# Kernel optimization log

Hardware: AMD Instinct MI355X
Metric: run time of the kernel (lower is better)

The kernel has to match this reference:

```python
import jax, jax.numpy as jnp
import numpy as np

B, S, D, H = 128, 512, 256, 256


def _lstm_cell(Wih, Whh, b, x_t, h, c):
    # PyTorch LSTM gate order: i, f, g, o. b = b_ih + b_hh (mathematically equivalent).
    z = x_t @ Wih.T + h @ Whh.T + b  # [B, 4H]
    i, f, g, o = jnp.split(z, 4, axis=-1)
    i = jax.nn.sigmoid(i)
    f = jax.nn.sigmoid(f)
    g = jnp.tanh(g)
    o = jax.nn.sigmoid(o)
    c = f * c + i * g
    h = o * jnp.tanh(c)
    return h, c


def setup_inputs() -> dict:
    key = jax.random.key(0)
    ks = jax.random.split(key, 12)
    s = 1.0 / np.sqrt(H)
    f32 = jnp.float32
    return {
        "x": jax.random.normal(ks[0], (B, S, D), f32),
        "enc_Wih": jax.random.uniform(ks[1], (4 * H, D), f32, -s, s),
        "enc_Whh": jax.random.uniform(ks[2], (4 * H, H), f32, -s, s),
        "enc_b": jax.random.uniform(ks[3], (4 * H,), f32, -s, s),
        "dec_Wih": jax.random.uniform(ks[4], (4 * H, D), f32, -s, s),
        "dec_Whh": jax.random.uniform(ks[5], (4 * H, H), f32, -s, s),
        "dec_b": jax.random.uniform(ks[6], (4 * H,), f32, -s, s),
        "W1_w": jax.random.uniform(ks[7], (H, H), f32, -s, s),
        "W1_b": jax.random.uniform(ks[8], (H,), f32, -s, s),
        "W2_w": jax.random.uniform(ks[9], (H, H), f32, -s, s),
        "W2_b": jax.random.uniform(ks[10], (H,), f32, -s, s),
        "vt_w": jax.random.uniform(ks[11], (H,), f32, -s, s),
    }


def reference(x, enc_Wih, enc_Whh, enc_b, dec_Wih, dec_Whh, dec_b,
              W1_w, W1_b, W2_w, W2_b, vt_w):
    b_, s_, d_ = x.shape
    h0 = jnp.zeros((b_, H), x.dtype)
    c0 = jnp.zeros((b_, H), x.dtype)

    # ---- encoder LSTM over time ----
    def enc_step(carry, x_t):
        h, c = carry
        h, c = _lstm_cell(enc_Wih, enc_Whh, enc_b, x_t, h, c)
        return (h, c), h

    (h, c), enc_out = jax.lax.scan(enc_step, (h0, c0), jnp.swapaxes(x, 0, 1))
    enc_out = jnp.swapaxes(enc_out, 0, 1)  # [B, S, H]

    # W1(encoder_outputs) is loop-invariant; compute once (same math as original)
    enc_proj = enc_out @ W1_w.T + W1_b  # [B, S, H]

    # ---- pointer decode loop ----
    def dec_step(carry, _):
        h, c, din = carry
        h, c = _lstm_cell(dec_Wih, dec_Whh, dec_b, din, h, c)
        q = h @ W2_w.T + W2_b  # [B, H]
        u = jnp.einsum('bsh,h->bs', jnp.tanh(enc_proj + q[:, None, :]), vt_w)
        probs = jax.nn.softmax(u, axis=1)  # [B, S]
        din = jnp.einsum('bs,bsh->bh', probs, enc_out)
        return (h, c, din), probs

    din0 = jnp.zeros((b_, d_), x.dtype)
    _, probs_seq = jax.lax.scan(dec_step, (h, c, din0), None, length=s_)
    return jnp.swapaxes(probs_seq, 0, 1)  # [B, S, S]
```

## Files before the change

kernel.cpp:

```cpp
#include <hip/hip_runtime.h>
#include <hip/hip_fp16.h>

typedef _Float16 h2_t __attribute__((ext_vector_type(2)));
typedef unsigned int u32x4 __attribute__((ext_vector_type(4)));

#define KEXP 2.8853900817779268f

#define BARRIER() do { \
    asm volatile("s_waitcnt lgkmcnt(0)" ::: "memory"); \
    __builtin_amdgcn_s_barrier(); \
    asm volatile("" ::: "memory"); \
} while (0)

__device__ __forceinline__ float fdot2(unsigned int a, unsigned int b, float c) {
#if __has_builtin(__builtin_amdgcn_fdot2)
    return __builtin_amdgcn_fdot2(__builtin_bit_cast(h2_t, a), __builtin_bit_cast(h2_t, b), c, false);
#else
    h2_t ha = __builtin_bit_cast(h2_t, a), hb = __builtin_bit_cast(h2_t, b);
    return c + (float)ha[0]*(float)hb[0] + (float)ha[1]*(float)hb[1];
#endif
}

__device__ __forceinline__ float dot4(u32x4 a, u32x4 b, float c) {
    c = fdot2(a[0], b[0], c); c = fdot2(a[1], b[1], c);
    c = fdot2(a[2], b[2], c); c = fdot2(a[3], b[3], c);
    return c;
}

__device__ __forceinline__ unsigned int pk16(float a, float b) {
    auto h = __builtin_amdgcn_cvt_pkrtz(a, b);
    return __builtin_bit_cast(unsigned int, h);
}

__device__ __forceinline__ float rcp_(float x) {
#if __has_builtin(__builtin_amdgcn_rcpf)
    return __builtin_amdgcn_rcpf(x);
#else
    return 1.0f / x;
#endif
}

__device__ __forceinline__ float sigm(float x) { return rcp_(1.0f + __expf(-x)); }
__device__ __forceinline__ float tanh_(float x) {
    float e = __expf(2.0f * x);
    return 1.0f - 2.0f * rcp_(e + 1.0f);
}

__device__ __forceinline__ unsigned int rcp1p2exp(unsigned int s) {
    __half2 e = h2exp2(__builtin_bit_cast(__half2, s));
    __half2 d = __hadd2(e, __float2half2_rn(1.0f));
    return __builtin_bit_cast(unsigned int, h2rcp(d));
}
__device__ __forceinline__ unsigned int hadd2u(unsigned int a, unsigned int b) {
    return __builtin_bit_cast(unsigned int,
        __hadd2(__builtin_bit_cast(__half2, a), __builtin_bit_cast(__half2, b)));
}

__device__ __forceinline__ void st_u32(unsigned int* p, unsigned int v) {
    __hip_atomic_store(p, v, __ATOMIC_RELAXED, __HIP_MEMORY_SCOPE_AGENT);
}
__device__ __forceinline__ unsigned int ld_u32(const unsigned int* p) {
    return __hip_atomic_load(p, __ATOMIC_RELAXED, __HIP_MEMORY_SCOPE_AGENT);
}
__device__ __forceinline__ float ld_f32(const unsigned int* p) {
    return __builtin_bit_cast(float, ld_u32(p));
}
__device__ __forceinline__ float h2f_lo(unsigned int v) {
    return __half2float(__ushort_as_half((unsigned short)(v & 0xffffu)));
}
__device__ __forceinline__ float h2f_hi(unsigned int v) {
    return __half2float(__ushort_as_half((unsigned short)(v >> 16)));
}

__global__ void init_flags_kernel(unsigned int* flags) {
    flags[threadIdx.x * 32] = 0u;
}

__global__ __launch_bounds__(256) void prep_kernel(
    const float* __restrict__ encWhh, const float* __restrict__ decWih,
    const float* __restrict__ decWhh, const float* __restrict__ W2w,
    u32x4* __restrict__ We8, u32x4* __restrict__ Wi8, u32x4* __restrict__ Wh8, u32x4* __restrict__ W28)
{
    int id = blockIdx.x * 256 + threadIdx.x;
    if (id < 3 * 32768) {
        int mat = id >> 15, local = id & 32767;
        int j = local & 1023, k8 = local >> 10;
        const float* src = mat == 0 ? encWhh : (mat == 1 ? decWih : decWhh);
        u32x4* dst = mat == 0 ? We8 : (mat == 1 ? Wi8 : Wh8);
        const float* p = src + (size_t)j * 256 + k8 * 8;
        float4 a = *(const float4*)p; float4 c = *(const float4*)(p + 4);
        u32x4 v; v[0] = pk16(a.x, a.y); v[1] = pk16(a.z, a.w);
        v[2] = pk16(c.x, c.y); v[3] = pk16(c.z, c.w);
        dst[k8 * 1024 + j] = v;
    } else {
        int local = id - 3 * 32768;
        if (local < 8192) {
            int m = local & 255, k8 = local >> 8;
            const float* p = W2w + (size_t)m * 256 + k8 * 8;
            float4 a = *(const float4*)p; float4 c = *(const float4*)(p + 4);
            u32x4 v; v[0] = pk16(a.x, a.y); v[1] = pk16(a.z, a.w);
            v[2] = pk16(c.x, c.y); v[3] = pk16(c.z, c.w);
            W28[k8 * 256 + m] = v;
        }
    }
}

template<int A_IS_F16, int TR_OUT>
__global__ __launch_bounds__(256) void gemm_kernel(
    const void* __restrict__ A_, const float* __restrict__ Bw,
    const float* __restrict__ bias, unsigned short* __restrict__ C, int N, float scale)
{
    __shared__ float As[16][68];
    __shared__ float Bs[16][132];
    const int t = threadIdx.x;
    const int row0 = blockIdx.y * 64, col0 = blockIdx.x * 128;
    const int ty = t >> 4, tx = t & 15;
    const int lm = t & 63, lkq = t >> 6;
    const int ln = t & 127, lkq2 = t >> 7;
    float acc[4][8] = {};
    for (int k0 = 0; k0 < 256; k0 += 16) {
        float4 av;
        if constexpr (A_IS_F16) {
            const unsigned short* A = (const unsigned short*)A_;
            uint2 ha = *(const uint2*)(A + (size_t)(row0 + lm) * 256 + k0 + lkq * 4);
            h2_t h0 = __builtin_bit_cast(h2_t, ha.x);
            h2_t h1 = __builtin_bit_cast(h2_t, ha.y);
            av = make_float4((float)h0[0], (float)h0[1], (float)h1[0], (float)h1[1]);
        } else {
            av = *(const float4*)((const float*)A_ + (size_t)(row0 + lm) * 256 + k0 + lkq * 4);
        }
        const float* bp = Bw + (size_t)(col0 + ln) * 256 + k0 + lkq2 * 8;
        float4 bv0 = *(const float4*)bp;
        float4 bv1 = *(const float4*)(bp + 4);
        __syncthreads();
        As[lkq * 4 + 0][lm] = av.x;
        As[lkq * 4 + 1][lm] = av.y;
        As[lkq * 4 + 2][lm] = av.z;
        As[lkq * 4 + 3][lm] = av.w;
        Bs[lkq2 * 8 + 0][ln] = bv0.x;
        Bs[lkq2 * 8 + 1][ln] = bv0.y;
        Bs[lkq2 * 8 + 2][ln] = bv0.z;
        Bs[lkq2 * 8 + 3][ln] = bv0.w;
        Bs[lkq2 * 8 + 4][ln] = bv1.x;
        Bs[lkq2 * 8 + 5][ln] = bv1.y;
        Bs[lkq2 * 8 + 6][ln] = bv1.z;
        Bs[lkq2 * 8 + 7][ln] = bv1.w;
        __syncthreads();
        #pragma unroll
        for (int kk = 0; kk < 16; ++kk) {
            float4 a = *(float4*)&As[kk][ty * 4];
            float4 b0 = *(float4*)&Bs[kk][tx * 8];
            float4 b1 = *(float4*)&Bs[kk][tx * 8 + 4];
            float ar[4] = {a.x, a.y, a.z, a.w};
            float br[8] = {b0.x, b0.y, b0.z, b0.w, b1.x, b1.y, b1.z, b1.w};
            #pragma unroll
            for (int i = 0; i < 4; ++i)
                #pragma unroll
                for (int j = 0; j < 8; ++j)
                    acc[i][j] = fmaf(ar[i], br[j], acc[i][j]);
        }
    }
    float bv[8];
    #pragma unroll
    for (int j = 0; j < 8; ++j) bv[j] = bias[col0 + tx * 8 + j];
    #pragma unroll
    for (int i = 0; i < 4; ++i) {
        unsigned int w0 = pk16((acc[i][0] + bv[0]) * scale, (acc[i][1] + bv[1]) * scale);
        unsigned int w1 = pk16((acc[i][2] + bv[2]) * scale, (acc[i][3] + bv[3]) * scale);
        unsigned int w2 = pk16((acc[i][4] + bv[4]) * scale, (acc[i][5] + bv[5]) * scale);
        unsigned int w3 = pk16((acc[i][6] + bv[6]) * scale, (acc[i][7] + bv[7]) * scale);
        uint4 val = make_uint4(w0, w1, w2, w3);
        if constexpr (TR_OUT) {
            int rr = row0 + ty * 4 + i;
            int bb = rr >> 9, s = rr & 511;
            int c8 = (col0 >> 3) + tx;
            ((uint4*)C)[(size_t)bb * 16384 + (size_t)c8 * 512 + s] = val;
        } else {
            *(uint4*)(C + (size_t)(row0 + ty * 4 + i) * N + col0 + tx * 8) = val;
        }
    }
}

__global__ __launch_bounds__(1024) void encoder_kernel(
    const unsigned short* __restrict__ Xproj, const u32x4* __restrict__ We8,
    float* __restrict__ hfin, float* __restrict__ cfin,
    unsigned short* __restrict__ enc_h, unsigned int* __restrict__ encT)
{
    const int b = blockIdx.x, t = threadIdx.x;
    __shared__ __align__(16) float zs[1024];
    __shared__ __align__(16) unsigned int hh2[128];
    if (t < 128) hh2[t] = 0u;
    float c_reg = 0.f, hprev = 0.f, hcur = 0.f;
    __syncthreads();
    const unsigned short* xp = Xproj + (size_t)b * 512 * 1024 + t;
    for (int step = 0; step < 512; ++step) {
        float acc = __half2float(__ushort_as_half(__builtin_nontemporal_load(xp)));
        #pragma unroll 8
        for (int k8 = 0; k8 < 32; ++k8) {
            u32x4 wv = We8[k8 * 1024 + t];
            u32x4 hv = *(const u32x4*)&hh2[k8 * 4];
            acc = dot4(wv, hv, acc);
        }
        zs[t] = acc;
        __syncthreads();
        if (t < 256) {
            float ig = sigm(zs[t]), fg = sigm(zs[t + 256]);
            float gg = tanh_(zs[t + 512]), og = sigm(zs[t + 768]);
            c_reg = fg * c_reg + ig * gg;
            float h = og * tanh_(c_reg);
            float hnb = __shfl_down(h, 1);
            if (!(t & 1)) hh2[t >> 1] = pk16(h, hnb);
            __builtin_nontemporal_store(__half_as_ushort(__float2half_rn(h)),
                                        enc_h + (size_t)(b * 512 + step) * 256 + t);
            if (step & 1) {
                int s2 = step >> 1;
                encT[(size_t)b * 65536 + (size_t)((s2 >> 2) * 256 + t) * 4 + (s2 & 3)] = pk16(hprev, h);
            }
            hprev = h; hcur = h;
        }
        __syncthreads();
        xp += 1024;
    }
    if (t < 256) { hfin[b * 256 + t] = hcur; cfin[b * 256 + t] = c_reg; }
}

__global__ __launch_bounds__(1024) void decoder_kernel(
    const u32x4* __restrict__ Wi8, const u32x4* __restrict__ Wh8, const u32x4* __restrict__ W28,
    const float* __restrict__ dec_b, const float* __restrict__ W2b, const float* __restrict__ vtw,
    const float* __restrict__ hfin, const float* __restrict__ cfin,
    const u32x4* __restrict__ projT, const u32x4* __restrict__ encT,
    unsigned int* __restrict__ xgate, unsigned int* __restrict__ xdin,
    unsigned int* __restrict__ xsum, unsigned int* __restrict__ flags,
    float* __restrict__ out)
{
    const int blk = blockIdx.x;
    const int b = blk & 127, r = blk >> 7;
    const int t = threadIdx.x;
    const int lane = t & 63, w = t >> 6;

    __shared__ __align__(16) float zs[1024];
    __shared__ __align__(16) unsigned int hh2[128];
    __shared__ __align__(16) unsigned int din2[128];
    __shared__ __align__(16) unsigned int qp2[128];
    __shared__ __align__(16) unsigned int mv2u[128];
    __shared__ __align__(16) unsigned int p2u[128];
    __shared__ float wreds[16];
    __shared__ float svtS, rsS;

    const int fo_me = (b * 2 + r) * 32, fo_pr = (b * 2 + (1 - r)) * 32;
    const int go_me = (b * 2 + r) * 256, go_pr = (b * 2 + (1 - r)) * 256;

    float c_reg = (t < 256) ? cfin[b * 256 + t] : 0.f;
    const float bja = (t < 256) ? dec_b[r * 512 + t] : 0.f;
    const float bjb = (t < 256) ? dec_b[r * 512 + 256 + t] : 0.f;
    const float w2b_r = (t < 256) ? W2b[t] : 0.f;
    if (t < 128) { din2[t] = 0u; mv2u[t] = pk16(-2.f * vtw[2 * t], -2.f * vtw[2 * t + 1]); }
    if (t < 256) zs[t] = vtw[t];
    __syncthreads();
    if (t < 64) {
        float v = zs[t] + zs[t + 64] + zs[t + 128] + zs[t + 192];
        #pragma unroll
        for (int off = 1; off < 64; off <<= 1) v += __shfl_xor(v, off);
        if (t == 0) svtS = v;
    }
    if (t < 256) {
        float h0 = hfin[b * 256 + t];
        float hnb = __shfl_down(h0, 1);
        if (!(t & 1)) hh2[t >> 1] = pk16(h0, hnb);
    }
    __syncthreads();
    const float svt = svtS;

    const int jl = t & 511, kh = t >> 9;
    const u32x4* wp = (kh ? Wh8 : Wi8) + (r * 512 + jl);
    const unsigned int* vls = kh ? (const unsigned int*)hh2 : (const unsigned int*)din2;
    const int hF = t & 255, slF = t >> 8;
    const int sl4 = t >> 2, qr = t & 3;
    const int s_g = r * 256 + sl4;
    const u32x4* pD = projT + (size_t)b * 16384 + (size_t)(qr * 8) * 512 + s_g;
    const u32x4* fD = encT + (size_t)b * 16384 + (size_t)(r * 32 + slF * 8) * 256 + hF;
    float* outp = out + (size_t)b * 262144;

    for (int step = 0; step < 512; ++step) {
        float acc = 0.f;
        #pragma unroll 8
        for (int k8 = 0; k8 < 32; ++k8) {
            u32x4 wv = wp[k8 * 1024];
            u32x4 hv = *(const u32x4*)&vls[k8 * 4];
            acc = dot4(wv, hv, acc);
        }
        zs[t] = acc;
        BARRIER();
        unsigned int myg = 0u;
        if (t < 256) {
            float z_a = bja + zs[t] + zs[t + 512];
            float z_b = bjb + zs[t + 256] + zs[t + 768];
            float ga, gb;
            if (r == 0) { ga = sigm(z_a); gb = sigm(z_b); }
            else        { ga = tanh_(z_a); gb = sigm(z_b); }
            myg = (unsigned int)__half_as_ushort(__float2half_rn(ga)) |
                  ((unsigned int)__half_as_ushort(__float2half_rn(gb)) << 16);
            st_u32(&xgate[go_me + t], myg);
            asm volatile("s_waitcnt vmcnt(0)" ::: "memory");
        }
        BARRIER();
        if (t == 0) {
            unsigned int T = (unsigned)(2 * step + 1);
            st_u32(&flags[fo_me], T);
            while (ld_u32(&flags[fo_pr]) < T) __builtin_amdgcn_s_sleep(1);
        }
        BARRIER();
        if (t < 256) {
            unsigned int og = ld_u32(&xgate[go_pr + t]);
            float la = h2f_lo(myg), lb = h2f_hi(myg);
            float oa = h2f_lo(og),  ob = h2f_hi(og);
            float gi, gf, gg, go_;
            if (r == 0) { gi = la; gf = lb; gg = oa; go_ = ob; }
            else        { gg = la; go_ = lb; gi = oa; gf = ob; }
            c_reg = gf * c_reg + gi * gg;
            float h = go_ * tanh_(c_reg);
            float hnb = __shfl_down(h, 1);
            if (!(t & 1)) hh2[t >> 1] = pk16(h, hnb);
        }
        BARRIER();
        {
            float qa = 0.f;
            #pragma unroll
            for (int i = 0; i < 8; ++i) {
                int k8 = slF * 8 + i;
                u32x4 wv = W28[k8 * 256 + hF];
                u32x4 hv = *(const u32x4*)&hh2[k8 * 4];
                qa = dot4(wv, hv, qa);
            }
            zs[t] = qa;
        }
        BARRIER();
        if (t < 256) {
            float q = (w2b_r + zs[t] + zs[t + 256] + zs[t + 512] + zs[t + 768]) * KEXP;
            float qnx = __shfl_down(q, 1);
            if (!(t & 1)) qp2[t >> 1] = pk16(q, qnx);
        }
        BARRIER();
        float e;
        u32x4 fv[8];
        {
            float up = 0.f;
            #pragma unroll 4
            for (int i = 0; i < 8; ++i) {
                u32x4 pv = pD[i * 512];
                int c = qr * 8 + i;
                u32x4 qh = *(const u32x4*)&qp2[c * 4];
                u32x4 mv = *(const u32x4*)&mv2u[c * 4];
                up = fdot2(mv[0], rcp1p2exp(hadd2u(pv[0], qh[0])), up);
                up = fdot2(mv[1], rcp1p2exp(hadd2u(pv[1], qh[1])), up);
                up = fdot2(mv[2], rcp1p2exp(hadd2u(pv[2], qh[2])), up);
                up = fdot2(mv[3], rcp1p2exp(hadd2u(pv[3], qh[3])), up);
            }
            up += __shfl_xor(up, 1);
            up += __shfl_xor(up, 2);
            e = __expf(up + svt);
            #pragma unroll
            for (int j = 0; j < 8; ++j) fv[j] = fD[j * 256];
            float enx = __shfl_down(e, 4);
            if (!(t & 7)) p2u[t >> 3] = pk16(e, enx);
            float ws = e;
            #pragma unroll
            for (int off = 1; off < 64; off <<= 1) ws += __shfl_xor(ws, off);
            if (lane == 0) wreds[w] = ws;
        }
        BARRIER();
        {
            float fa = 0.f;
            #pragma unroll
            for (int j = 0; j < 8; ++j) {
                u32x4 ev = fv[j];
                u32x4 pw = *(const u32x4*)&p2u[(slF * 8 + j) * 4];
                fa = dot4(ev, pw, fa);
            }
            zs[t] = fa;
        }
        BARRIER();
        float dpart = 0.f;
        if (t < 256) {
            dpart = zs[t] + zs[t + 256] + zs[t + 512] + zs[t + 768];
            st_u32(&xdin[go_me + t], __builtin_bit_cast(unsigned int, dpart));
            asm volatile("s_waitcnt vmcnt(0)" ::: "memory");
        }
        BARRIER();
        if (t == 0) {
            float ls = 0.f;
            #pragma unroll
            for (int k = 0; k < 16; ++k) ls += wreds[k];
            ls *= 0.25f;
            st_u32(&xsum[fo_me], __builtin_bit_cast(unsigned int, ls));
            asm volatile("s_waitcnt vmcnt(0)" ::: "memory");
            unsigned int T = (unsigned)(2 * step + 2);
            st_u32(&flags[fo_me], T);
            while (ld_u32(&flags[fo_pr]) < T) __builtin_amdgcn_s_sleep(1);
            float lr = __builtin_bit_cast(float, ld_u32(&xsum[fo_pr]));
            rsS = rcp_(ls + lr);
        }
        BARRIER();
        {
            float rs = rsS;
            if (t < 256) {
                float drem = __builtin_bit_cast(float, ld_u32(&xdin[go_pr + t]));
                float dval = (dpart + drem) * rs;
                float dnx = __shfl_down(dval, 1);
                if (!(t & 1)) din2[t >> 1] = pk16(dval, dnx);
            }
            if ((t & 3) == 0) outp[(size_t)step * 512 + s_g] = e * rs;
        }
        BARRIER();
    }
}

extern "C" void kernel_launch(void* const* d_in, const int* in_sizes, int n_in,
                              void* d_out, int out_size, void* d_ws, size_t ws_size,
                              hipStream_t stream) {
    const float* x      = (const float*)d_in[0];
    const float* encWih = (const float*)d_in[1];
    const float* encWhh = (const float*)d_in[2];
    const float* enc_b  = (const float*)d_in[3];
    const float* decWih = (const float*)d_in[4];
    const float* decWhh = (const float*)d_in[5];
    const float* dec_bp = (const float*)d_in[6];
    const float* W1w    = (const float*)d_in[7];
    const float* W1b    = (const float*)d_in[8];
    const float* W2w    = (const float*)d_in[9];
    const float* W2bp   = (const float*)d_in[10];
    const float* vtw    = (const float*)d_in[11];

    char* ws = (char*)d_ws;
    u32x4* We8 = (u32x4*)(ws);
    u32x4* Wi8 = (u32x4*)(ws + 524288);
    u32x4* Wh8 = (u32x4*)(ws + 1048576);
    u32x4* W28 = (u32x4*)(ws + 1572864);
    unsigned short* enc_h = (unsigned short*)(ws + 1703936);
    unsigned int*   encT  = (unsigned int*)(ws + 35258368);
    unsigned short* projT = (unsigned short*)(ws + 68812800);
    float* hfin = (float*)(ws + 102367232);
    float* cfin = (float*)(ws + 102498304);

    unsigned int* flags = (unsigned int*)(ws + 1703936);
    unsigned int* xsum  = (unsigned int*)(ws + 1703936 + 32768);
    unsigned int* xgate = (unsigned int*)(ws + 1703936 + 65536);
    unsigned int* xdin  = (unsigned int*)(ws + 1703936 + 65536 + 262144);

    unsigned short* Xproj = (unsigned short*)d_out;

    prep_kernel<<<416, 256, 0, stream>>>(encWhh, decWih, decWhh, W2w, We8, Wi8, Wh8, W28);
    gemm_kernel<0, 0><<<dim3(8, 1024), 256, 0, stream>>>(x, encWih, enc_b, Xproj, 1024, 1.0f);
    encoder_kernel<<<128, 1024, 0, stream>>>(Xproj, We8, hfin, cfin, enc_h, (unsigned int*)encT);
    gemm_kernel<1, 1><<<dim3(2, 1024), 256, 0, stream>>>(enc_h, W1w, W1b, projT, 256, KEXP);
    init_flags_kernel<<<1, 256, 0, stream>>>(flags);
    decoder_kernel<<<256, 1024, 0, stream>>>(Wi8, Wh8, W28, dec_bp, W2bp, vtw,
                                             hfin, cfin, (const u32x4*)projT, (const u32x4*)encT,
                                             xgate, xdin, xsum, flags, (float*)d_out);
}
```

Baseline: 13.86 ms.

## Split encoder LSTM across two cooperating blocks per batch with flag exchange

The encoder now runs two workgroups per batch element. Each owns half of the gate outputs, and each thread reduces half of the hidden dimension, with partial sums combined in shared memory. The two blocks trade activated gate halves through global memory every step, using per-step flags and spin-waits, and split the enc_h and encT output writes between them. This halves the per-block weight streaming and per-step matvec latency of the serial recurrence. In exchange it adds a cross-block global handshake on every timestep and depends on both blocks being co-resident.

```diff
diff --git a/kernel.cpp b/kernel.cpp
--- a/kernel.cpp
+++ b/kernel.cpp
@@ -184,44 +184,79 @@
 __global__ __launch_bounds__(1024) void encoder_kernel(
     const unsigned short* __restrict__ Xproj, const u32x4* __restrict__ We8,
     float* __restrict__ hfin, float* __restrict__ cfin,
-    unsigned short* __restrict__ enc_h, unsigned int* __restrict__ encT)
+    unsigned short* __restrict__ enc_h, unsigned int* __restrict__ encT,
+    unsigned int* __restrict__ xg, unsigned int* __restrict__ eflags)
 {
-    const int b = blockIdx.x, t = threadIdx.x;
+    const int blk = blockIdx.x;
+    const int b = blk & 127, r = blk >> 7;
+    const int t = threadIdx.x;
     __shared__ __align__(16) float zs[1024];
     __shared__ __align__(16) unsigned int hh2[128];
     if (t < 128) hh2[t] = 0u;
     float c_reg = 0.f, hprev = 0.f, hcur = 0.f;
     __syncthreads();
-    const unsigned short* xp = Xproj + (size_t)b * 512 * 1024 + t;
+
+    const int jl = t & 511, kh = t >> 9;
+    const u32x4* wp = We8 + (size_t)(kh * 16) * 1024 + r * 512 + jl;
+    const unsigned short* xp = Xproj + (size_t)b * 524288 + r * 512 + jl;
+    const int fo_me = (b * 2 + r) * 32, fo_pr = (b * 2 + (1 - r)) * 32;
+    unsigned int* xg_me = xg + (b * 2 + r) * 512;
+    const unsigned int* xg_pr = xg + (b * 2 + (1 - r)) * 512;
+
     for (int step = 0; step < 512; ++step) {
-        float acc = __half2float(__ushort_as_half(__builtin_nontemporal_load(xp)));
+        float acc = (kh == 0)
+            ? __half2float(__ushort_as_half(__builtin_nontemporal_load(xp + (size_t)step * 1024)))
+            : 0.f;
         #pragma unroll 8
-        for (int k8 = 0; k8 < 32; ++k8) {
-            u32x4 wv = We8[k8 * 1024 + t];
-            u32x4 hv = *(const u32x4*)&hh2[k8 * 4];
+        for (int i = 0; i < 16; ++i) {
+            u32x4 wv = wp[i * 1024];
+            u32x4 hv = *(const u32x4*)&hh2[(kh * 16 + i) * 4];
             acc = dot4(wv, hv, acc);
         }
         zs[t] = acc;
-        __syncthreads();
+        BARRIER();
+        float ga = 0.f, gb = 0.f;
         if (t < 256) {
-            float ig = sigm(zs[t]), fg = sigm(zs[t + 256]);
-            float gg = tanh_(zs[t + 512]), og = sigm(zs[t + 768]);
-            c_reg = fg * c_reg + ig * gg;
-            float h = og * tanh_(c_reg);
+            float z_a = zs[t] + zs[t + 512];
+            float z_b = zs[t + 256] + zs[t + 768];
+            if (r == 0) { ga = sigm(z_a); gb = sigm(z_b); }
+            else        { ga = tanh_(z_a); gb = sigm(z_b); }
+            st_u32(&xg_me[t], __builtin_bit_cast(unsigned int, ga));
+            st_u32(&xg_me[256 + t], __builtin_bit_cast(unsigned int, gb));
+            asm volatile("s_waitcnt vmcnt(0)" ::: "memory");
+        }
+        BARRIER();
+        if (t == 0) {
+            unsigned int T = (unsigned)(step + 1);
+            st_u32(&eflags[fo_me], T);
+            while (ld_u32(&eflags[fo_pr]) < T) __builtin_amdgcn_s_sleep(1);
+        }
+        BARRIER();
+        if (t < 256) {
+            float oa = ld_f32(&xg_pr[t]);
+            float ob = ld_f32(&xg_pr[256 + t]);
+            float gi, gf, gg, go_;
+            if (r == 0) { gi = ga; gf = gb; gg = oa; go_ = ob; }
+            else        { gg = ga; go_ = gb; gi = oa; gf = ob; }
+            c_reg = gf * c_reg + gi * gg;
+            float h = go_ * tanh_(c_reg);
             float hnb = __shfl_down(h, 1);
             if (!(t & 1)) hh2[t >> 1] = pk16(h, hnb);
-            __builtin_nontemporal_store(__half_as_ushort(__float2half_rn(h)),
-                                        enc_h + (size_t)(b * 512 + step) * 256 + t);
-            if (step & 1) {
-                int s2 = step >> 1;
-                encT[(size_t)b * 65536 + (size_t)((s2 >> 2) * 256 + t) * 4 + (s2 & 3)] = pk16(hprev, h);
+            if (r == 0) {
+                __builtin_nontemporal_store(__half_as_ushort(__float2half_rn(h)),
+                                            enc_h + (size_t)(b * 512 + step) * 256 + t);
+            } else {
+                if (step & 1) {
+                    int s2 = step >> 1;
+                    encT[(size_t)b * 65536 + (size_t)((s2 >> 2) * 256 + t) * 4 + (s2 & 3)] = pk16(hprev, h);
+                }
+                hprev = h;
             }
-            hprev = h; hcur = h;
-        }
-        __syncthreads();
-        xp += 1024;
-    }
-    if (t < 256) { hfin[b * 256 + t] = hcur; cfin[b * 256 + t] = c_reg; }
+            hcur = h;
+        }
+        BARRIER();
+    }
+    if (r == 0 && t < 256) { hfin[b * 256 + t] = hcur; cfin[b * 256 + t] = c_reg; }
 }
 
 __global__ __launch_bounds__(1024) void decoder_kernel(
@@ -447,11 +482,16 @@
     unsigned int* xgate = (unsigned int*)(ws + 1703936 + 65536);
     unsigned int* xdin  = (unsigned int*)(ws + 1703936 + 65536 + 262144);
 
+    unsigned int* eflags = (unsigned int*)(ws + 68812800);
+    unsigned int* exg    = (unsigned int*)(ws + 68812800 + 32768);
+
     unsigned short* Xproj = (unsigned short*)d_out;
 
     prep_kernel<<<416, 256, 0, stream>>>(encWhh, decWih, decWhh, W2w, We8, Wi8, Wh8, W28);
     gemm_kernel<0, 0><<<dim3(8, 1024), 256, 0, stream>>>(x, encWih, enc_b, Xproj, 1024, 1.0f);
-    encoder_kernel<<<128, 1024, 0, stream>>>(Xproj, We8, hfin, cfin, enc_h, (unsigned int*)encT);
+    init_flags_kernel<<<1, 256, 0, stream>>>(eflags);
+    encoder_kernel<<<256, 1024, 0, stream>>>(Xproj, We8, hfin, cfin, enc_h, (unsigned int*)encT,
+                                             exg, eflags);
     gemm_kernel<1, 1><<<dim3(2, 1024), 256, 0, stream>>>(enc_h, W1w, W1b, projT, 256, KEXP);
     init_flags_kernel<<<1, 256, 0, stream>>>(flags);
     decoder_kernel<<<256, 1024, 0, stream>>>(Wi8, Wh8, W28, dec_bp, W2bp, vtw,
```

Result: no change. 13.73 ms (-0.9%).
